# Kernel tuning notes

Measured on AMD Instinct MI355X. Metric: run time of the kernel, lower is better.

The kernel has to match this reference:

```python
import jax, jax.numpy as jnp
import numpy as np

N = 50000   # nodes
E = 800000  # edges (avg degree 16)
F = 128     # node_features


def setup_inputs() -> dict:
    key = jax.random.key(0)
    ks = jax.random.split(key, 10)
    s = 1.0 / np.sqrt(F)
    x = jax.random.normal(ks[0], (N, F), jnp.float32)
    edge_index = jax.random.randint(ks[1], (2, E), 0, N, dtype=jnp.int32)
    edge_weight = jax.random.uniform(ks[2], (E,), jnp.float32)
    # EvolveGCNO initial weight (glorot-ish) and GRU parameters (PyTorch layout)
    W0 = jax.random.uniform(ks[3], (F, F), jnp.float32, -s, s)
    W_ih = jax.random.uniform(ks[4], (3 * F, F), jnp.float32, -s, s)
    W_hh = jax.random.uniform(ks[5], (3 * F, F), jnp.float32, -s, s)
    b_ih = jax.random.uniform(ks[6], (3 * F,), jnp.float32, -s, s)
    b_hh = jax.random.uniform(ks[7], (3 * F,), jnp.float32, -s, s)
    # Linear(F, 1) head
    w_lin = jax.random.uniform(ks[8], (1, F), jnp.float32, -s, s)
    b_lin = jax.random.uniform(ks[9], (1,), jnp.float32, -s, s)
    return dict(x=x, edge_index=edge_index, edge_weight=edge_weight, W0=W0,
                W_ih=W_ih, W_hh=W_hh, b_ih=b_ih, b_hh=b_hh,
                w_lin=w_lin, b_lin=b_lin)


def _gru_evolve(W0, W_ih, W_hh, b_ih, b_hh):
    # GRU(input=W0, hidden=W0): seq_len=1, batch=F, feature=F (PyTorch gate order r,z,n)
    gi = W0 @ W_ih.T + b_ih  # [F, 3F]
    gh = W0 @ W_hh.T + b_hh  # [F, 3F]
    f = W0.shape[1]
    i_r, i_z, i_n = gi[:, :f], gi[:, f:2 * f], gi[:, 2 * f:]
    h_r, h_z, h_n = gh[:, :f], gh[:, f:2 * f], gh[:, 2 * f:]
    r = jax.nn.sigmoid(i_r + h_r)
    z = jax.nn.sigmoid(i_z + h_z)
    n = jnp.tanh(i_n + r * h_n)
    return (1.0 - z) * n + z * W0  # evolved weight [F, F]


def reference(x, edge_index, edge_weight, W0, W_ih, W_hh, b_ih, b_hh, w_lin, b_lin):
    n_nodes = x.shape[0]
    W = _gru_evolve(W0, W_ih, W_hh, b_ih, b_hh)
    # gcn_norm: add self loops (weight 1), symmetric D^-1/2 A D^-1/2
    loop = jnp.arange(n_nodes, dtype=edge_index.dtype)
    src = jnp.concatenate([edge_index[0], loop])
    dst = jnp.concatenate([edge_index[1], loop])
    w = jnp.concatenate([edge_weight, jnp.ones((n_nodes,), x.dtype)])
    deg = jax.ops.segment_sum(w, dst, num_segments=n_nodes)
    dinv = jnp.where(deg > 0, jax.lax.rsqrt(deg), 0.0)
    norm = dinv[src] * w * dinv[dst]  # [E+N]
    xw = x @ W  # [N, F]
    h = jax.ops.segment_sum(norm[:, None] * xw[src], dst, num_segments=n_nodes)
    h = jnp.tanh(h)
    return h @ w_lin.T + b_lin  # [N, 1]
```

## Files before the change

kernel.cpp:

```cpp
#include <hip/hip_runtime.h>
#include <hip/hip_bf16.h>
#include <math.h>

#define N_NODES 50000
#define N_EDGES 800000
#define FDIM 128
#define XW_BLOCKS 391
#define HIST_BLOCKS 782
#define MAXDEG 64

typedef unsigned int uint32;
typedef __attribute__((ext_vector_type(8))) __bf16 bf16x8;
typedef __attribute__((ext_vector_type(8))) short short8;
typedef __attribute__((ext_vector_type(16))) float f32x16;

__device__ inline unsigned short f2bf(float f) {
  unsigned int u = __float_as_uint(f);
  unsigned int r = u + 0x7fffu + ((u >> 16) & 1u);
  return (unsigned short)(r >> 16);
}

__global__ __launch_bounds__(384) void evolve_kernel(
    const float* __restrict__ W0, const float* __restrict__ Wih,
    const float* __restrict__ Whh, const float* __restrict__ bih,
    const float* __restrict__ bhh, unsigned short* __restrict__ Wbf,
    int* __restrict__ cnt) {
  int i = blockIdx.x;
  int jj = threadIdx.x;
  int gid = i * 384 + jj;
  for (int j = gid; j < N_NODES; j += 128 * 384) cnt[j] = 0;

  __shared__ float w0s[FDIM];
  __shared__ float gis[3 * FDIM];
  __shared__ float ghs[3 * FDIM];
  if (jj < FDIM) w0s[jj] = W0[i * FDIM + jj];
  __syncthreads();
  float gi = bih[jj], gh = bhh[jj];
  const float4* wih4 = (const float4*)(Wih + jj * FDIM);
  const float4* whh4 = (const float4*)(Whh + jj * FDIM);
#pragma unroll 8
  for (int k = 0; k < FDIM / 4; k++) {
    float4 a = wih4[k];
    float4 b = whh4[k];
    float w0a = w0s[4 * k], w0b = w0s[4 * k + 1];
    float w0c = w0s[4 * k + 2], w0d = w0s[4 * k + 3];
    gi += a.x * w0a + a.y * w0b + a.z * w0c + a.w * w0d;
    gh += b.x * w0a + b.y * w0b + b.z * w0c + b.w * w0d;
  }
  gis[jj] = gi;
  ghs[jj] = gh;
  __syncthreads();
  if (jj < FDIM) {
    float r = 1.0f / (1.0f + expf(-(gis[jj] + ghs[jj])));
    float z = 1.0f / (1.0f + expf(-(gis[jj + FDIM] + ghs[jj + FDIM])));
    float nn = tanhf(gis[jj + 2 * FDIM] + r * ghs[jj + 2 * FDIM]);
    float val = (1.0f - z) * nn + z * w0s[jj];
    Wbf[((((i >> 3) << 7) + jj) << 3) + (i & 7)] = f2bf(val);
  }
}

__global__ __launch_bounds__(256) void histxw_kernel(
    const int* __restrict__ ei, const float* __restrict__ ew,
    int* __restrict__ cnt, int2* __restrict__ csr, const float* __restrict__ x,
    const unsigned short* __restrict__ Wbf, unsigned short* __restrict__ y,
    int n) {
  __shared__ short Bs[8192];
  int t = threadIdx.x;
  if (blockIdx.x >= XW_BLOCKS) {
    int e0 = (blockIdx.x - XW_BLOCKS) * 1024 + t * 4;
    if (e0 < N_EDGES) {
      int4 d4 = *(const int4*)(ei + N_EDGES + e0);
      int4 s4 = *(const int4*)(ei + e0);
      float4 w4 = *(const float4*)(ew + e0);
      int r0 = atomicAdd(&cnt[d4.x], 1);
      int r1 = atomicAdd(&cnt[d4.y], 1);
      int r2 = atomicAdd(&cnt[d4.z], 1);
      int r3 = atomicAdd(&cnt[d4.w], 1);
      if (r0 < MAXDEG)
        csr[d4.x * MAXDEG + r0] = make_int2(s4.x, __float_as_int(w4.x));
      if (r1 < MAXDEG)
        csr[d4.y * MAXDEG + r1] = make_int2(s4.y, __float_as_int(w4.y));
      if (r2 < MAXDEG)
        csr[d4.z * MAXDEG + r2] = make_int2(s4.z, __float_as_int(w4.z));
      if (r3 < MAXDEG)
        csr[d4.w * MAXDEG + r3] = make_int2(s4.w, __float_as_int(w4.w));
    }
    return;
  }
  int lane = t & 63;
  int wid = blockIdx.x * 4 + (t >> 6);
  int tr = wid * 32;
  int m = lane & 31;
  int q2 = lane >> 5;

  int row = tr + m;
  if (row >= n) row = n - 1;
  const float* xr = x + (size_t)row * FDIM;

  bf16x8 a[8];
#pragma unroll
  for (int kc = 0; kc < 8; kc++) {
    int k0 = kc * 16 + q2 * 8;
    float4 p = *(const float4*)(xr + k0);
    float4 q = *(const float4*)(xr + k0 + 4);
    short8 s;
    s[0] = (short)f2bf(p.x); s[1] = (short)f2bf(p.y);
    s[2] = (short)f2bf(p.z); s[3] = (short)f2bf(p.w);
    s[4] = (short)f2bf(q.x); s[5] = (short)f2bf(q.y);
    s[6] = (short)f2bf(q.z); s[7] = (short)f2bf(q.w);
    a[kc] = __builtin_bit_cast(bf16x8, s);
  }

  f32x16 acc[4];
#pragma unroll
  for (int ct = 0; ct < 4; ct++) {
#pragma unroll
    for (int r = 0; r < 16; r++) acc[ct][r] = 0.0f;
  }

#pragma unroll
  for (int h = 0; h < 2; h++) {
    __syncthreads();
#pragma unroll
    for (int i = 0; i < 4; i++) {
      int li = i * 256 + t;
      ((short8*)Bs)[li] =
          ((const short8*)Wbf)[((li >> 6) << 7) + (h << 6) + (li & 63)];
    }
    __syncthreads();
#pragma unroll
    for (int cti = 0; cti < 2; cti++) {
      int ct = h * 2 + cti;
      int nnl = cti * 32 + m;
#pragma unroll
      for (int kc = 0; kc < 8; kc++) {
        int kg = kc * 2 + q2;
        bf16x8 b = __builtin_bit_cast(bf16x8,
                                      ((const short8*)Bs)[(kg << 6) + nnl]);
        acc[ct] = __builtin_amdgcn_mfma_f32_32x32x16_bf16(a[kc], b, acc[ct],
                                                          0, 0, 0);
      }
    }
  }

#pragma unroll
  for (int r = 0; r < 16; r++) {
    int rl = (r & 3) + ((r >> 2) << 3) + (q2 << 2);
    int rg = tr + rl;
    if (rg < n) {
#pragma unroll
      for (int ct = 0; ct < 4; ct++) {
        y[(size_t)rg * FDIM + ct * 32 + m] = f2bf(acc[ct][r]);
      }
    }
  }
}

__global__ __launch_bounds__(256) void deg_dinv_kernel(
    const int2* __restrict__ csr, const int* __restrict__ cnt,
    float* __restrict__ dinv, int n) {
  int i = blockIdx.x * blockDim.x + threadIdx.x;
  if (i >= n) return;
  int c = cnt[i];
  if (c > MAXDEG) c = MAXDEG;
  const int2* row = csr + i * MAXDEG;
  float d = 1.0f;
  for (int j = 0; j < c; j++) d += __int_as_float(row[j].y);
  dinv[i] = (d > 0.0f) ? rsqrtf(d) : 0.0f;
}

__global__ __launch_bounds__(256) void gather_kernel(
    const uint4* __restrict__ yb4, const int* __restrict__ cnt,
    const int2* __restrict__ csr, const float* __restrict__ dinv,
    const float* __restrict__ wl, const float* __restrict__ bl,
    float* __restrict__ out, int n) {
  int wid = (int)((blockIdx.x * (size_t)blockDim.x + threadIdx.x) >> 6);
  int lane = threadIdx.x & 63;
  if (wid >= n) return;
  int g = lane >> 4;
  int d = lane & 15;
  float di = dinv[wid];

  uint4 sv = yb4[(size_t)wid * 16 + d];
  float selfw = (g == 0) ? di : 0.0f;
  float acc[8];
  acc[0] = selfw * __uint_as_float(sv.x << 16);
  acc[1] = selfw * __uint_as_float(sv.x & 0xffff0000u);
  acc[2] = selfw * __uint_as_float(sv.y << 16);
  acc[3] = selfw * __uint_as_float(sv.y & 0xffff0000u);
  acc[4] = selfw * __uint_as_float(sv.z << 16);
  acc[5] = selfw * __uint_as_float(sv.z & 0xffff0000u);
  acc[6] = selfw * __uint_as_float(sv.w << 16);
  acc[7] = selfw * __uint_as_float(sv.w & 0xffff0000u);

  int mm = cnt[wid];
  if (mm > MAXDEG) mm = MAXDEG;
  int base = wid * MAXDEG;
  int cx = wid;
  float wn_l = 0.0f;
  if (lane < mm) {
    int2 c = csr[base + lane];
    cx = c.x;
    wn_l = __int_as_float(c.y) * dinv[c.x];
  }
  int ng = (mm + 3) >> 2;
  int j = 0;
  for (; j + 2 <= ng; j += 2) {
    int sl0 = j * 4 + g, sl1 = sl0 + 4;
    int r0 = __shfl(cx, sl0);
    int r1 = __shfl(cx, sl1);
    float w0 = __shfl(wn_l, sl0);
    float w1 = __shfl(wn_l, sl1);
    uint4 u0 = yb4[(size_t)r0 * 16 + d];
    uint4 u1 = yb4[(size_t)r1 * 16 + d];
    acc[0] += w0 * __uint_as_float(u0.x << 16);
    acc[1] += w0 * __uint_as_float(u0.x & 0xffff0000u);
    acc[2] += w0 * __uint_as_float(u0.y << 16);
    acc[3] += w0 * __uint_as_float(u0.y & 0xffff0000u);
    acc[4] += w0 * __uint_as_float(u0.z << 16);
    acc[5] += w0 * __uint_as_float(u0.z & 0xffff0000u);
    acc[6] += w0 * __uint_as_float(u0.w << 16);
    acc[7] += w0 * __uint_as_float(u0.w & 0xffff0000u);
    acc[0] += w1 * __uint_as_float(u1.x << 16);
    acc[1] += w1 * __uint_as_float(u1.x & 0xffff0000u);
    acc[2] += w1 * __uint_as_float(u1.y << 16);
    acc[3] += w1 * __uint_as_float(u1.y & 0xffff0000u);
    acc[4] += w1 * __uint_as_float(u1.z << 16);
    acc[5] += w1 * __uint_as_float(u1.z & 0xffff0000u);
    acc[6] += w1 * __uint_as_float(u1.w << 16);
    acc[7] += w1 * __uint_as_float(u1.w & 0xffff0000u);
  }
  if (j < ng) {
    int sl = j * 4 + g;
    int r0 = __shfl(cx, sl);
    float w0 = __shfl(wn_l, sl);
    uint4 u0 = yb4[(size_t)r0 * 16 + d];
    acc[0] += w0 * __uint_as_float(u0.x << 16);
    acc[1] += w0 * __uint_as_float(u0.x & 0xffff0000u);
    acc[2] += w0 * __uint_as_float(u0.y << 16);
    acc[3] += w0 * __uint_as_float(u0.y & 0xffff0000u);
    acc[4] += w0 * __uint_as_float(u0.z << 16);
    acc[5] += w0 * __uint_as_float(u0.z & 0xffff0000u);
    acc[6] += w0 * __uint_as_float(u0.w << 16);
    acc[7] += w0 * __uint_as_float(u0.w & 0xffff0000u);
  }

#pragma unroll
  for (int k = 0; k < 8; k++) {
    acc[k] += __shfl_xor(acc[k], 16, 64);
    acc[k] += __shfl_xor(acc[k], 32, 64);
  }

  const float4* wl4 = (const float4*)wl;
  float4 wa = wl4[d * 2], wb = wl4[d * 2 + 1];
  float p = tanhf(di * acc[0]) * wa.x + tanhf(di * acc[1]) * wa.y +
            tanhf(di * acc[2]) * wa.z + tanhf(di * acc[3]) * wa.w +
            tanhf(di * acc[4]) * wb.x + tanhf(di * acc[5]) * wb.y +
            tanhf(di * acc[6]) * wb.z + tanhf(di * acc[7]) * wb.w;
#pragma unroll
  for (int o = 1; o < 16; o <<= 1) p += __shfl_xor(p, o, 64);
  if (lane == 0) out[wid] = p + bl[0];
}

extern "C" void kernel_launch(void* const* d_in, const int* in_sizes, int n_in,
                              void* d_out, int out_size, void* d_ws,
                              size_t ws_size, hipStream_t stream) {
  const float* x = (const float*)d_in[0];
  const int* ei = (const int*)d_in[1];
  const float* ew = (const float*)d_in[2];
  const float* W0 = (const float*)d_in[3];
  const float* Wih = (const float*)d_in[4];
  const float* Whh = (const float*)d_in[5];
  const float* bih = (const float*)d_in[6];
  const float* bhh = (const float*)d_in[7];
  const float* wl = (const float*)d_in[8];
  const float* bl = (const float*)d_in[9];
  float* out = (float*)d_out;

  unsigned short* Wbf = (unsigned short*)d_ws;
  unsigned short* y = Wbf + 16384;
  float* dinv = (float*)(y + (size_t)N_NODES * FDIM);
  int* cnt = (int*)(dinv + N_NODES);
  int2* csr = (int2*)(cnt + N_NODES);

  evolve_kernel<<<FDIM, 384, 0, stream>>>(W0, Wih, Whh, bih, bhh, Wbf, cnt);
  histxw_kernel<<<XW_BLOCKS + HIST_BLOCKS, 256, 0, stream>>>(ei, ew, cnt, csr,
                                                             x, Wbf, y,
                                                             N_NODES);
  deg_dinv_kernel<<<(N_NODES + 255) / 256, 256, 0, stream>>>(csr, cnt, dinv,
                                                             N_NODES);
  gather_kernel<<<(N_NODES * 64) / 256, 256, 0, stream>>>(
      (const uint4*)y, cnt, csr, dinv, wl, bl, out, N_NODES);
}
```

Baseline: 191.4 us.

## Split edge histogram and CSR scatter into separate kernels via rank buffer

The histogram blocks now only perform the atomic count per destination and store the returned rank to a new per-edge buffer. A separate scatter kernel afterwards reads source, weight, destination and rank and writes the CSR slots. The aim is to take the dependent scattered writes off the atomic-return latency path inside the fused kernel, where they run alongside the xW MFMA blocks. In exchange it adds an extra kernel launch, a rank buffer written and read back, and a second read of the edge arrays.

```diff
diff --git a/kernel.cpp b/kernel.cpp
--- a/kernel.cpp
+++ b/kernel.cpp
@@ -60,30 +60,20 @@
 }
 
 __global__ __launch_bounds__(256) void histxw_kernel(
-    const int* __restrict__ ei, const float* __restrict__ ew,
-    int* __restrict__ cnt, int2* __restrict__ csr, const float* __restrict__ x,
-    const unsigned short* __restrict__ Wbf, unsigned short* __restrict__ y,
-    int n) {
+    const int* __restrict__ ei, int* __restrict__ cnt, int* __restrict__ rank,
+    const float* __restrict__ x, const unsigned short* __restrict__ Wbf,
+    unsigned short* __restrict__ y, int n) {
   __shared__ short Bs[8192];
   int t = threadIdx.x;
   if (blockIdx.x >= XW_BLOCKS) {
     int e0 = (blockIdx.x - XW_BLOCKS) * 1024 + t * 4;
     if (e0 < N_EDGES) {
       int4 d4 = *(const int4*)(ei + N_EDGES + e0);
-      int4 s4 = *(const int4*)(ei + e0);
-      float4 w4 = *(const float4*)(ew + e0);
       int r0 = atomicAdd(&cnt[d4.x], 1);
       int r1 = atomicAdd(&cnt[d4.y], 1);
       int r2 = atomicAdd(&cnt[d4.z], 1);
       int r3 = atomicAdd(&cnt[d4.w], 1);
-      if (r0 < MAXDEG)
-        csr[d4.x * MAXDEG + r0] = make_int2(s4.x, __float_as_int(w4.x));
-      if (r1 < MAXDEG)
-        csr[d4.y * MAXDEG + r1] = make_int2(s4.y, __float_as_int(w4.y));
-      if (r2 < MAXDEG)
-        csr[d4.z * MAXDEG + r2] = make_int2(s4.z, __float_as_int(w4.z));
-      if (r3 < MAXDEG)
-        csr[d4.w * MAXDEG + r3] = make_int2(s4.w, __float_as_int(w4.w));
+      *(int4*)(rank + e0) = make_int4(r0, r1, r2, r3);
     }
     return;
   }
@@ -153,6 +143,27 @@
         y[(size_t)rg * FDIM + ct * 32 + m] = f2bf(acc[ct][r]);
       }
     }
+  }
+}
+
+__global__ __launch_bounds__(256) void scatter_kernel(
+    const int* __restrict__ ei, const float* __restrict__ ew,
+    const int* __restrict__ rank, int2* __restrict__ csr) {
+  int idx = blockIdx.x * blockDim.x + threadIdx.x;
+  int e0 = idx * 4;
+  if (e0 < N_EDGES) {
+    int4 s4 = *(const int4*)(ei + e0);
+    int4 d4 = *(const int4*)(ei + N_EDGES + e0);
+    float4 w4 = *(const float4*)(ew + e0);
+    int4 r4 = *(const int4*)(rank + e0);
+    if (r4.x < MAXDEG)
+      csr[d4.x * MAXDEG + r4.x] = make_int2(s4.x, __float_as_int(w4.x));
+    if (r4.y < MAXDEG)
+      csr[d4.y * MAXDEG + r4.y] = make_int2(s4.y, __float_as_int(w4.y));
+    if (r4.z < MAXDEG)
+      csr[d4.z * MAXDEG + r4.z] = make_int2(s4.z, __float_as_int(w4.z));
+    if (r4.w < MAXDEG)
+      csr[d4.w * MAXDEG + r4.w] = make_int2(s4.w, __float_as_int(w4.w));
   }
 }
 
@@ -281,12 +292,13 @@
   unsigned short* y = Wbf + 16384;
   float* dinv = (float*)(y + (size_t)N_NODES * FDIM);
   int* cnt = (int*)(dinv + N_NODES);
-  int2* csr = (int2*)(cnt + N_NODES);
+  int* rank = cnt + N_NODES;
+  int2* csr = (int2*)(rank + N_EDGES);
 
   evolve_kernel<<<FDIM, 384, 0, stream>>>(W0, Wih, Whh, bih, bhh, Wbf, cnt);
-  histxw_kernel<<<XW_BLOCKS + HIST_BLOCKS, 256, 0, stream>>>(ei, ew, cnt, csr,
-                                                             x, Wbf, y,
-                                                             N_NODES);
+  histxw_kernel<<<XW_BLOCKS + HIST_BLOCKS, 256, 0, stream>>>(ei, cnt, rank, x,
+                                                             Wbf, y, N_NODES);
+  scatter_kernel<<<HIST_BLOCKS, 256, 0, stream>>>(ei, ew, rank, csr);
   deg_dinv_kernel<<<(N_NODES + 255) / 256, 256, 0, stream>>>(csr, cnt, dinv,
                                                              N_NODES);
   gather_kernel<<<(N_NODES * 64) / 256, 256, 0, stream>>>(
```

Measured after the change: 189.8 us. Within noise of the previous version (-0.8%).
